# Kernel tuning notes

Measured on AMD Instinct MI355X. Metric: run time of the kernel, lower is better.

## Reference

```python
import jax, jax.numpy as jnp
import numpy as np

B, S, H, DK, DV, DE = 2, 256, 8, 64, 64, 512
DT = H * DV
EPS = 1e-5

def _clin(xr, xi, W, b):
    # complex linear: x @ W + b with (re, im) parts; W: (2, d_in, d_out), b: (2, d_out)
    yr = xr @ W[0] - xi @ W[1] + b[0]
    yi = xr @ W[1] + xi @ W[0] + b[1]
    return yr, yi

def _emul(ar, ai, br, bi):
    # complex elementwise (Hadamard) multiply
    return ar * br - ai * bi, ar * bi + ai * br

def _forward(Z_q, Z_k, Z_v, t_measure_all, Wq, bq, Wk, bk, Wv, bv, Wp, bp,
             lambda_imag_v, lambda_real_v, lambda_omega_sqrt_v,
             lambda_gamma_sqrt_v, noise_floor, tau, eta_param):
    Bn = Z_q.shape[0]
    t = t_measure_all[0, :-1]
    t = t / (t[-1] - t[0])

    def heads(z, W, b, d):
        yr, yi = _clin(z[:, 0], z[:, 1], W, b)
        f = lambda a: a.reshape(Bn, S, H, d).swapaxes(-1, -2)  # (B,S,d,H)
        return f(yr), f(yi)

    Qr, Qi = heads(Z_q, Wq, bq, DK)
    Kr, Ki = heads(Z_k, Wk, bk, DK)
    Vr, Vi = heads(Z_v, Wv, bv, DV)

    # complex eigenvalues in conjugate pairs: (DV, H)
    lam_im = jnp.concatenate([lambda_imag_v, -lambda_imag_v], axis=1).T
    lam_re = jnp.broadcast_to(lambda_real_v[None, :], (DV, H))

    # forward/backward exponential kernels exp(+/- lambda t): (S, DV, H)
    phase = t[:, None, None] * lam_im[None]
    mag = jnp.exp(t[:, None, None] * lam_re[None])
    ef_r = mag * jnp.cos(phase); ef_i = mag * jnp.sin(phase)
    eb_r = jnp.cos(phase) / mag; eb_i = -jnp.sin(phase) / mag
    me_r, me_i = ef_r[0], ef_i[0]  # mat_exp

    # scalar covariance kernel per (i, j, head): process noise + measurement noise
    omega = lambda_omega_sqrt_v ** 2
    gamma = lambda_gamma_sqrt_v ** 2 + EPS
    dt = jnp.maximum(t[:, None] - t[None, :], 0.0)  # causal lags only
    den = 2.0 * lambda_real_v  # (H,)
    safe = jnp.where(jnp.abs(den) > 1e-6, den, 1.0)
    x = dt[:, :, None] * den
    g = jnp.where(jnp.abs(den) > 1e-6, jnp.expm1(x) / safe, dt[:, :, None])
    V_avg = omega * g + gamma * jnp.exp(x)  # (S,S,H)

    # factorized kernels: U_* = exp(-lambda t_j) * X_j ; propagator factor |exp(lambda t_i)|^2
    Uq_r, Uq_i = _emul(eb_r[None], eb_i[None], Qr, Qi)
    Uk_r, Uk_i = _emul(eb_r[None], eb_i[None], Kr, Ki)
    Uv_r, Uv_i = _emul(eb_r[None], eb_i[None], Vr, Vi)
    Vk2 = ef_r ** 2 + ef_i ** 2  # (S,DV,H)

    # precision-weighted residual norm |exp(lambda(t_i-t_j)) k_j - q_i|^2
    Uq2 = Uq_r ** 2 + Uq_i ** 2
    Uk2 = Uk_r ** 2 + Uk_i ** 2
    self_q = jnp.einsum('idh,bidh->bih', Vk2, Uq2)
    term_k = jnp.einsum('idh,bjdh->bijh', Vk2, Uk2)
    cross = (jnp.einsum('bidh,bjdh->bijh', Vk2[None] * Uq_r, Uk_r)
             + jnp.einsum('bidh,bjdh->bijh', Vk2[None] * Uq_i, Uk_i))
    R = term_k + self_q[:, :, None, :] - 2.0 * cross  # (B,S,S,H)

    base = (noise_floor ** 2 + EPS) * V_avg[None] + R
    scores = -(tau ** 2) * jnp.log(base)
    mask = jnp.tril(jnp.ones((S, S), bool))
    scores = jnp.where(mask[None, :, :, None], scores, -jnp.inf)
    attn = jax.nn.softmax(scores, axis=2)  # (B,S,S,H)

    # complex matmul with real-valued attention (imag part of Q_ij is zero)
    er = jnp.einsum('bijh,bjdh->bidh', attn, Uv_r)
    ei = jnp.einsum('bijh,bjdh->bidh', attn, Uv_i)
    est_r, est_i = _emul(ef_r[None], ef_i[None], er, ei)

    eta = jax.nn.sigmoid(eta_param)[0, 0]  # (1,DV,H)
    el_r = (1.0 - eta) * Vr + jax.nn.sigmoid(eta) * est_r
    el_i = (1.0 - eta) * Vi + jax.nn.sigmoid(eta) * est_i

    pr, pi = _emul(me_r[None, None], me_i[None, None], el_r, el_i)
    merge = lambda a: a.swapaxes(-1, -2).reshape(Bn, S, DT)
    o_r, o_i = _clin(merge(pr), merge(pi), Wp, bp)
    out = jnp.stack([o_r, o_i], axis=1)  # (B,2,S,DE)

    # all-pairs propagated estimates Z_ij = exp(lambda t_i) * U_v,j
    zr, zi = _emul(ef_r[None, :, None], ef_i[None, :, None],
                   Uv_r[:, None], Uv_i[:, None])  # (B,S,S,DV,H)
    zm = lambda a: a.swapaxes(-1, -2).reshape(Bn, S, S, DT)
    Z_ij = jnp.stack([zm(zr), zm(zi)], axis=1)  # (B,2,S,S,DT)

    est_latent = jnp.stack([el_r, el_i], axis=1)  # (B,2,S,DV,H)
    Q_ij = jnp.stack([attn, jnp.zeros_like(attn)], axis=1)
    epoch_lambdas = jnp.stack([lam_re, lam_im], 0).swapaxes(-1, -2).reshape(2, H * DV)[..., None]
    return est_latent, out, Q_ij, Z_ij, epoch_lambdas

def setup_inputs():
    key = jax.random.key(0)
    k = jax.random.split(key, 16)
    sc_in = 1.0 / np.sqrt(DE)
    sc_out = 1.0 / np.sqrt(DT)
    return {
        'Z_q': jax.random.normal(k[0], (B, 2, S, DE), jnp.float32),
        'Z_k': jax.random.normal(k[1], (B, 2, S, DE), jnp.float32),
        'Z_v': jax.random.normal(k[2], (B, 2, S, DE), jnp.float32),
        't_measure_all': jnp.arange(S + 1, dtype=jnp.float32)[None, :],
        'Wq': jax.random.normal(k[3], (2, DE, DT), jnp.float32) * sc_in,
        'bq': jax.random.normal(k[4], (2, DT), jnp.float32) * 0.01,
        'Wk': jax.random.normal(k[5], (2, DE, DT), jnp.float32) * sc_in,
        'bk': jax.random.normal(k[6], (2, DT), jnp.float32) * 0.01,
        'Wv': jax.random.normal(k[7], (2, DE, DT), jnp.float32) * sc_in,
        'bv': jax.random.normal(k[8], (2, DT), jnp.float32) * 0.01,
        'Wp': jax.random.normal(k[9], (2, DT, DE), jnp.float32) * sc_out,
        'bp': jax.random.normal(k[10], (2, DE), jnp.float32) * 0.01,
        'lambda_imag_v': jax.random.normal(k[11], (H, DV // 2), jnp.float32),
        'lambda_real_v': jax.random.normal(k[12], (H,), jnp.float32) * 0.5,
        'lambda_omega_sqrt_v': jax.random.normal(k[13], (H,), jnp.float32),
        'lambda_gamma_sqrt_v': jax.random.normal(k[14], (H,), jnp.float32),
        'noise_floor': jnp.ones((H,), jnp.float32),
        'tau': jnp.ones((H,), jnp.float32),
        'eta_param': jnp.zeros((1, 1, 1, DV, H), jnp.float32),
    }

def reference(Z_q, Z_k, Z_v, t_measure_all, Wq, bq, Wk, bk, Wv, bv, Wp, bp,
              lambda_imag_v, lambda_real_v, lambda_omega_sqrt_v,
              lambda_gamma_sqrt_v, noise_floor, tau, eta_param):
    return _forward(Z_q, Z_k, Z_v, t_measure_all, Wq, bq, Wk, bk, Wv, bv, Wp, bp,
                    lambda_imag_v, lambda_real_v, lambda_omega_sqrt_v,
                    lambda_gamma_sqrt_v, noise_floor, tau, eta_param)
```

## Files before the change

kernel.cpp:

```cpp
#include <hip/hip_runtime.h>
#include <hip/hip_bf16.h>
#include <math.h>

constexpr int kB  = 2;
constexpr int kS  = 256;
constexpr int kH  = 8;
constexpr float kEPS = 1e-5f;

constexpr int OFF_EST = 0;
constexpr int OFF_OUT = 524288;
constexpr int OFF_QIJ = 1048576;
constexpr int OFF_ZIJ = 3145728;
constexpr int OFF_EPO = 137363456;

constexpr int WS_EFR = 0;
constexpr int WS_EFI = 131072;
constexpr int WS_EBR = 262144;
constexpr int WS_EBI = 393216;
constexpr int WS_UQR = 524288;
constexpr int WS_UQI = 786432;
constexpr int WS_UKR = 1048576;
constexpr int WS_UKI = 1310720;
constexpr int WS_UVR = 1572864;
constexpr int WS_UVI = 1835008;
constexpr int WS_VR  = 2097152;
constexpr int WS_VI  = 2359296;
constexpr int WS_BF  = 3145728;

constexpr int A2Q = 0;
constexpr int A2K = 524288;
constexpr int A2V = 1048576;
constexpr int B2R0 = 1572864;

typedef __attribute__((ext_vector_type(8))) short bf16x8;
typedef __attribute__((ext_vector_type(4))) float f32x4;
typedef __attribute__((ext_vector_type(8))) unsigned short u16x8;
typedef __attribute__((ext_vector_type(4))) unsigned short u16x4;

__device__ __forceinline__ float sigm(float x) { return 1.f / (1.f + expf(-x)); }
__device__ __forceinline__ unsigned short f2b(float f) {
    __hip_bfloat16 h = __float2bfloat16(f);
    return *reinterpret_cast<unsigned short*>(&h);
}

__global__ __launch_bounds__(256) void k_prep(
    const float* __restrict__ tall, const float* __restrict__ Lim,
    const float* __restrict__ Lre,
    const float* __restrict__ zq, const float* __restrict__ zk,
    const float* __restrict__ zv,
    const float* __restrict__ wq, const float* __restrict__ wk,
    const float* __restrict__ wv, const float* __restrict__ wp,
    float* __restrict__ efr, float* __restrict__ efi,
    float* __restrict__ ebr, float* __restrict__ ebi,
    float* __restrict__ epo, __hip_bfloat16* __restrict__ bfbase)
{
    __shared__ float s0[64][65];
    __shared__ float s1[64][65];
    const int bid = blockIdx.x;
    const int tid = threadIdx.x;

    if (bid < 512) {
        int idx = bid * 256 + tid;
        int s = idx >> 9;
        int c = idx & 511;
        int h = c >> 6;
        int d = c & 63;
        float li = (d < 32) ? Lim[h * 32 + d] : -Lim[h * 32 + d - 32];
        float lr = Lre[h];
        float t  = tall[s] / (tall[kS - 1] - tall[0]);
        float ph  = t * li;
        float mag = expf(t * lr);
        float cp  = cosf(ph);
        float sp  = sinf(ph);
        efr[idx] = mag * cp;
        efi[idx] = mag * sp;
        ebr[idx] = cp / mag;
        ebi[idx] = -sp / mag;
        if (s == 0) {
            epo[c]       = lr;
            epo[512 + c] = li;
        }
    } else if (bid < 1280) {
        int idx = (bid - 512) * 256 + tid;
        int tz  = idx >> 16;
        int rem = idx & 65535;
        int m   = rem >> 7;
        int k0  = (rem & 127) * 8;
        const float* src = (tz == 0) ? zq : (tz == 1) ? zk : zv;
        int b = m >> 8, s = m & 255;
        int c = (k0 >= 512) ? 1 : 0;
        int e = k0 - c * 512;
        const float* p = src + ((b * 2 + c) * 256 + s) * 512 + e;
        float4 v0 = *(const float4*)p;
        float4 v1 = *(const float4*)(p + 4);
        u16x8 o;
        o[0] = f2b(v0.x); o[1] = f2b(v0.y); o[2] = f2b(v0.z); o[3] = f2b(v0.w);
        o[4] = f2b(v1.x); o[5] = f2b(v1.y); o[6] = f2b(v1.z); o[7] = f2b(v1.w);
        __hip_bfloat16* dst = bfbase + ((tz == 0) ? A2Q : (tz == 1) ? A2K : A2V)
                              + m * 1024 + k0;
        *(u16x8*)dst = o;
    } else {
        int wid = bid - 1280;
        int z = wid >> 7;
        int r2 = wid & 127;
        int k0 = (r2 & 15) * 64;
        int n0 = (r2 >> 4) * 64;
        const float* W  = (z == 0) ? wq : (z == 1) ? wk : (z == 2) ? wv : wp;
        const float* W0 = W;
        const float* W1 = W + 262144;
        const int kp = k0 & 511;
        const bool hf = (k0 >= 512);
        const int r = tid >> 2;
        const int q = tid & 3;
#pragma unroll
        for (int c = 0; c < 4; ++c) {
            int col = q * 16 + c * 4;
            *(float4*)&s0[r][col] = *(const float4*)&W0[(kp + r) * 512 + n0 + col];
            *(float4*)&s1[r][col] = *(const float4*)&W1[(kp + r) * 512 + n0 + col];
        }
        __syncthreads();
        u16x8 r0, r1, i0, i1;
#pragma unroll
        for (int u = 0; u < 8; ++u) {
            int kl = q * 16 + u;
            float w0 = s0[kl][r], w1 = s1[kl][r];
            r0[u] = f2b(hf ? -w1 : w0);
            i0[u] = f2b(hf ?  w0 : w1);
        }
#pragma unroll
        for (int u = 0; u < 8; ++u) {
            int kl = q * 16 + 8 + u;
            float w0 = s0[kl][r], w1 = s1[kl][r];
            r1[u] = f2b(hf ? -w1 : w0);
            i1[u] = f2b(hf ?  w0 : w1);
        }
        __hip_bfloat16* pr = bfbase + B2R0 + z * 1048576
                             + (size_t)(n0 + r) * 1024 + k0 + q * 16;
        __hip_bfloat16* pi = pr + 524288;
        *(u16x8*)pr       = r0;
        *(u16x8*)(pr + 8) = r1;
        *(u16x8*)pi       = i0;
        *(u16x8*)(pi + 8) = i1;
    }
}

template<bool IS_P>
__global__ __launch_bounds__(256) void k_cmfma(
    const __hip_bfloat16* __restrict__ bfbase,
    const __hip_bfloat16* __restrict__ a2p,
    const float* __restrict__ bq, const float* __restrict__ bk,
    const float* __restrict__ bv, const float* __restrict__ bp,
    const float* __restrict__ ebr, const float* __restrict__ ebi,
    float* __restrict__ uqr, float* __restrict__ uqi,
    float* __restrict__ ukr, float* __restrict__ uki,
    float* __restrict__ uvr, float* __restrict__ uvi,
    float* __restrict__ vr,  float* __restrict__ vi,
    float* __restrict__ outp)
{
    __shared__ __align__(16) char sm[24576];
    char* sA  = sm;
    char* sBr = sm + 8192;
    char* sBi = sm + 16384;

    const int mode = IS_P ? 3 : (int)blockIdx.z;
    const __hip_bfloat16* A2 = IS_P ? a2p
        : bfbase + ((mode == 0) ? A2Q : (mode == 1) ? A2K : A2V);
    const __hip_bfloat16* Br = bfbase + B2R0 + mode * 1048576;
    const __hip_bfloat16* Bi = Br + 524288;
    const float* bias = IS_P ? bp : ((mode == 0) ? bq : (mode == 1) ? bk : bv);

    const int tid = threadIdx.x;
    const int m0 = blockIdx.y * 64;
    const int n0 = blockIdx.x * 64;
    const int lane = tid & 63;
    const int wv2 = tid >> 6;
    const int wr = wv2 >> 1, wc = wv2 & 1;
    const int lx = lane & 15, lhi = lane >> 4;

    const int srow  = tid >> 2;
    const int sslot = (tid & 3) * 32;

    const char* gA  = (const char*)(A2 + (size_t)(m0 + srow) * 1024);
    const char* gBr = (const char*)(Br + (size_t)(n0 + srow) * 1024);
    const char* gBi = (const char*)(Bi + (size_t)(n0 + srow) * 1024);
    const int swz = (srow & 7) << 4;
    char* dA  = sA  + srow * 128;
    char* dBr = sBr + srow * 128;
    char* dBi = sBi + srow * 128;

    f32x4 accR[2][2] = {};
    f32x4 accI[2][2] = {};

    int rowA[2], rowB[2];
    rowA[0] = wr * 32 + lx;  rowA[1] = rowA[0] + 16;
    rowB[0] = wc * 32 + lx;  rowB[1] = rowB[0] + 16;

    for (int kt = 0; kt < 16; ++kt) {
        const int kb = kt * 128;
        {
            float4 a0 = *(const float4*)(gA  + kb + sslot);
            float4 a1 = *(const float4*)(gA  + kb + sslot + 16);
            float4 b0 = *(const float4*)(gBr + kb + sslot);
            float4 b1 = *(const float4*)(gBr + kb + sslot + 16);
            float4 c0 = *(const float4*)(gBi + kb + sslot);
            float4 c1 = *(const float4*)(gBi + kb + sslot + 16);
            *(float4*)(dA  + ( sslot       ^ swz)) = a0;
            *(float4*)(dA  + ((sslot + 16) ^ swz)) = a1;
            *(float4*)(dBr + ( sslot       ^ swz)) = b0;
            *(float4*)(dBr + ((sslot + 16) ^ swz)) = b1;
            *(float4*)(dBi + ( sslot       ^ swz)) = c0;
            *(float4*)(dBi + ((sslot + 16) ^ swz)) = c1;
        }
        __syncthreads();
#pragma unroll
        for (int kk = 0; kk < 2; ++kk) {
            const int kbyte = kk * 64 + lhi * 16;
            bf16x8 af[2], brf[2], bif[2];
#pragma unroll
            for (int x = 0; x < 2; ++x) {
                int ra = rowA[x];
                af[x]  = *(const bf16x8*)(sA  + ra * 128 + (kbyte ^ ((ra & 7) << 4)));
                int rb = rowB[x];
                brf[x] = *(const bf16x8*)(sBr + rb * 128 + (kbyte ^ ((rb & 7) << 4)));
                bif[x] = *(const bf16x8*)(sBi + rb * 128 + (kbyte ^ ((rb & 7) << 4)));
            }
#pragma unroll
            for (int a = 0; a < 2; ++a)
#pragma unroll
                for (int bb = 0; bb < 2; ++bb) {
                    accR[a][bb] = __builtin_amdgcn_mfma_f32_16x16x32_bf16(
                        af[a], brf[bb], accR[a][bb], 0, 0, 0);
                    accI[a][bb] = __builtin_amdgcn_mfma_f32_16x16x32_bf16(
                        af[a], bif[bb], accI[a][bb], 0, 0, 0);
                }
        }
        __syncthreads();
    }

#pragma unroll
    for (int a = 0; a < 2; ++a) {
#pragma unroll
        for (int bb = 0; bb < 2; ++bb) {
#pragma unroll
            for (int j = 0; j < 4; ++j) {
                int m = m0 + wr * 32 + a * 16 + lhi * 4 + j;
                int n = n0 + wc * 32 + bb * 16 + lx;
                float yr = accR[a][bb][j] + bias[n];
                float yi = accI[a][bb][j] + bias[512 + n];
                int b = m >> 8, s = m & 255;
                if (IS_P) {
                    int rowo = m * 512 + b * 131072;
                    outp[rowo + n] = yr;
                    outp[rowo + 131072 + n] = yi;
                } else {
                    int h = n >> 6, d = n & 63;
                    float er_ = ebr[s * 512 + n], ei_ = ebi[s * 512 + n];
                    float ur = er_ * yr - ei_ * yi;
                    float ui = er_ * yi + ei_ * yr;
                    if (mode == 0) {
                        int idx = ((b * 8 + h) * 256 + s) * 64 + d;
                        uqr[idx] = ur; uqi[idx] = ui;
                    } else if (mode == 1) {
                        int idx = ((b * 8 + h) * 64 + d) * 256 + s;
                        ukr[idx] = ur; uki[idx] = ui;
                    } else {
                        int idx = ((b * 8 + h) * 256 + s) * 64 + d;
                        uvr[idx] = ur; uvi[idx] = ui;
                        int vidx = (b * 256 + s) * 512 + d * 8 + h;
                        vr[vidx] = yr; vi[vidx] = yi;
                    }
                }
            }
        }
    }
}

__global__ __launch_bounds__(256) void k_zij_attn(
    const float* __restrict__ efr, const float* __restrict__ efi,
    const float* __restrict__ uvr, const float* __restrict__ uvi,
    float* __restrict__ zout,
    const float* __restrict__ uqr, const float* __restrict__ uqi,
    const float* __restrict__ ukr, const float* __restrict__ uki,
    const float* __restrict__ tall,
    const float* __restrict__ Lre, const float* __restrict__ Lom,
    const float* __restrict__ Lga, const float* __restrict__ NF,
    const float* __restrict__ TAU,
    float* __restrict__ qij,
    const float* __restrict__ vr,  const float* __restrict__ vi,
    const float* __restrict__ ETA,
    float* __restrict__ out_est, __hip_bfloat16* __restrict__ a2p)
{
    __shared__ __align__(16) char smem[66688];
    float (*sP)[257] = (float(*)[257])smem;
    float (*sKr)[32] = (float(*)[32])(smem + 32896);
    float (*sKi)[32] = (float(*)[32])(smem + 41088);
    float (*sQr)[68] = (float(*)[68])(smem + 49280);
    float (*sQi)[68] = (float(*)[68])(smem + 57984);
    float (*sVr)[64] = (float(*)[64])(smem + 32896);
    float (*sVi)[64] = (float(*)[64])(smem + 41088);

    const int bid = blockIdx.x;
    const int tid = threadIdx.x;

    if (bid >= 128) {
        const int z  = bid - 128;
        const int j0 = (z & 63) * 4;
        const int i  = (z >> 6) & 255;
        const int b  = z >> 14;
#pragma unroll
        for (int half = 0; half < 2; half++) {
            int dt = half * 256 + tid;
            float fr = efr[i * 512 + dt];
            float fi = efi[i * 512 + dt];
            int h = dt >> 6, d = dt & 63;
            const float* ur = uvr + ((b * 8 + h) * 256) * 64 + d;
            const float* ui = uvi + ((b * 8 + h) * 256) * 64 + d;
#pragma unroll
            for (int jj = 0; jj < 4; jj++) {
                int j = j0 + jj;
                float vr_ = ur[j * 64];
                float vi_ = ui[j * 64];
                float zr = fr * vr_ - fi * vi_;
                float zi = fr * vi_ + fi * vr_;
                int idx0 = (b * 2) * 33554432 + i * 131072 + j * 512 + dt;
                __builtin_nontemporal_store(zr, &zout[idx0]);
                __builtin_nontemporal_store(zi, &zout[idx0 + 33554432]);
            }
        }
        return;
    }

    const int it = bid & 7;
    const int h  = (bid >> 3) & 7;
    const int b  = bid >> 6;
    const int i0 = it * 32;
    const int ti = tid >> 3;
    const int tj = tid & 7;
    const int i  = i0 + ti;

    {
        const float* qsr = uqr + ((b * 8 + h) * 256 + i) * 64;
        const float* qsi = uqi + ((b * 8 + h) * 256 + i) * 64;
        *(float4*)&sQr[ti][tj * 4]      = *(const float4*)&qsr[tj * 4];
        *(float4*)&sQr[ti][32 + tj * 4] = *(const float4*)&qsr[32 + tj * 4];
        *(float4*)&sQi[ti][tj * 4]      = *(const float4*)&qsi[tj * 4];
        *(float4*)&sQi[ti][32 + tj * 4] = *(const float4*)&qsi[32 + tj * 4];
    }

    const float lre  = Lre[h];
    const float om   = Lom[h] * Lom[h];
    const float ga   = Lga[h] * Lga[h] + kEPS;
    const float nf2  = NF[h] * NF[h] + kEPS;
    const float tau2 = TAU[h] * TAU[h];
    const float den  = 2.f * lre;
    const float invT = 1.f / (tall[kS - 1] - tall[0]);
    const float t_i  = tall[i] * invT;
    const float m2i  = expf(2.f * t_i * lre);
    const bool  denok = fabsf(den) > 1e-6f;

    const int kr2 = tid >> 2;
    const int kq2 = tid & 3;

    for (int jt = 0; jt <= it; ++jt) {
        const int j0 = jt * 32;
        __syncthreads();
        {
            const float* ksrc_r = ukr + ((b * 8 + h) * 64 + kr2) * 256 + j0;
            const float* ksrc_i = uki + ((b * 8 + h) * 64 + kr2) * 256 + j0;
            *(float4*)&sKr[kr2][kq2 * 4]      = *(const float4*)&ksrc_r[kq2 * 4];
            *(float4*)&sKr[kr2][16 + kq2 * 4] = *(const float4*)&ksrc_r[16 + kq2 * 4];
            *(float4*)&sKi[kr2][kq2 * 4]      = *(const float4*)&ksrc_i[kq2 * 4];
            *(float4*)&sKi[kr2][16 + kq2 * 4] = *(const float4*)&ksrc_i[16 + kq2 * 4];
        }
        __syncthreads();

        float acc[4] = {0.f, 0.f, 0.f, 0.f};
#pragma unroll 16
        for (int d = 0; d < 64; d++) {
            float qr = sQr[ti][d];
            float qi = sQi[ti][d];
            float4 kr = *(float4*)&sKr[d][tj * 4];
            float4 ki = *(float4*)&sKi[d][tj * 4];
#define DSTEP(c, KRC, KIC)                                    \
            { float dr = qr - KRC; float di = qi - KIC;       \
              acc[c] = fmaf(dr, dr, acc[c]);                  \
              acc[c] = fmaf(di, di, acc[c]); }
            DSTEP(0, kr.x, ki.x)
            DSTEP(1, kr.y, ki.y)
            DSTEP(2, kr.z, ki.z)
            DSTEP(3, kr.w, ki.w)
#undef DSTEP
        }

#pragma unroll
        for (int c = 0; c < 4; c++) {
            int j = j0 + tj * 4 + c;
            if (j <= i) {
                float t_j = tall[j] * invT;
                float dtt = fmaxf(t_i - t_j, 0.f);
                float x = dtt * den;
                float g = denok ? (expm1f(x) / den) : dtt;
                float Vv = om * g + ga * expf(x);
                float base = nf2 * Vv + m2i * acc[c];
                sP[ti][j] = -tau2 * logf(base);
            }
        }
    }
    __syncthreads();

    float mx = -1e30f;
    for (int j = tj; j <= i; j += 8) mx = fmaxf(mx, sP[ti][j]);
#pragma unroll
    for (int m = 1; m < 8; m <<= 1) mx = fmaxf(mx, __shfl_xor(mx, m));
    float sum = 0.f;
    for (int j = tj; j <= i; j += 8) {
        float e = expf(sP[ti][j] - mx);
        sP[ti][j] = e;
        sum += e;
    }
#pragma unroll
    for (int m = 1; m < 8; m <<= 1) sum += __shfl_xor(sum, m);
    const float inv = 1.f / sum;

    float* srow   = qij + ((b * 512 + i) * 256) * 8 + h;
    float* qi_out = qij + ((b * 512 + 256 + i) * 256) * 8 + h;
    const int jfill = i0 + 32;
    for (int j = tj; j < 256; j += 8) {
        float p = 0.f;
        if (j <= i) p = sP[ti][j] * inv;
        if (j < jfill) sP[ti][j] = p;
        srow[j * 8]   = p;
        qi_out[j * 8] = 0.f;
    }
    __syncthreads();

    const int dl = tid & 7;
    float accR[8] = {0.f}, accI[8] = {0.f};

    for (int jt = 0; jt <= it; jt++) {
        const int j0 = jt * 32;
        {
            const float* sr = uvr + ((b * 8 + h) * 256 + j0 + ti) * 64;
            const float* si = uvi + ((b * 8 + h) * 256 + j0 + ti) * 64;
            *(float4*)&sVr[ti][dl * 4]      = *(const float4*)&sr[dl * 4];
            *(float4*)&sVr[ti][32 + dl * 4] = *(const float4*)&sr[32 + dl * 4];
            *(float4*)&sVi[ti][dl * 4]      = *(const float4*)&si[dl * 4];
            *(float4*)&sVi[ti][32 + dl * 4] = *(const float4*)&si[32 + dl * 4];
        }
        __syncthreads();

#pragma unroll 8
        for (int jj = 0; jj < 32; jj++) {
            float a = sP[ti][j0 + jj];
            float4 v0 = *(float4*)&sVr[jj][dl * 8];
            float4 v1 = *(float4*)&sVr[jj][dl * 8 + 4];
            float4 w0 = *(float4*)&sVi[jj][dl * 8];
            float4 w1 = *(float4*)&sVi[jj][dl * 8 + 4];
            float vv[8] = {v0.x, v0.y, v0.z, v0.w, v1.x, v1.y, v1.z, v1.w};
            float ww[8] = {w0.x, w0.y, w0.z, w0.w, w1.x, w1.y, w1.z, w1.w};
#pragma unroll
            for (int c = 0; c < 8; c++) {
                accR[c] = fmaf(a, vv[c], accR[c]);
                accI[c] = fmaf(a, ww[c], accI[c]);
            }
        }
        __syncthreads();
    }

    const int cb = h * 64 + dl * 8;
    f32x4 fr0 = *(const f32x4*)&efr[i * 512 + cb];
    f32x4 fr1 = *(const f32x4*)&efr[i * 512 + cb + 4];
    f32x4 fi0 = *(const f32x4*)&efi[i * 512 + cb];
    f32x4 fi1 = *(const f32x4*)&efi[i * 512 + cb + 4];
    f32x4 mr0 = *(const f32x4*)&efr[cb];
    f32x4 mr1 = *(const f32x4*)&efr[cb + 4];
    f32x4 mi0 = *(const f32x4*)&efi[cb];
    f32x4 mi1 = *(const f32x4*)&efi[cb + 4];

    u16x8 o_r, o_i;
#pragma unroll
    for (int c = 0; c < 8; c++) {
        float fr = (c < 4) ? fr0[c] : fr1[c - 4];
        float fi = (c < 4) ? fi0[c] : fi1[c - 4];
        float mr = (c < 4) ? mr0[c] : mr1[c - 4];
        float mi = (c < 4) ? mi0[c] : mi1[c - 4];
        int p = dl * 64 + c * 8 + h;
        float estr = fr * accR[c] - fi * accI[c];
        float esti = fr * accI[c] + fi * accR[c];
        float et = sigm(ETA[p]);
        float w1 = 1.f - et;
        float w2 = sigm(et);
        float vr_ = vr[(b * 256 + i) * 512 + p];
        float vi_ = vi[(b * 256 + i) * 512 + p];
        float elr = w1 * vr_ + w2 * estr;
        float eli = w1 * vi_ + w2 * esti;
        out_est[((b * 2 + 0) * 256 + i) * 512 + p] = elr;
        out_est[((b * 2 + 1) * 256 + i) * 512 + p] = eli;
        o_r[c] = f2b(mr * elr - mi * eli);
        o_i[c] = f2b(mr * eli + mi * elr);
    }
    __hip_bfloat16* ap = a2p + (b * 256 + i) * 1024 + cb;
    *(u16x8*)ap         = o_r;
    *(u16x8*)(ap + 512) = o_i;
}

extern "C" void kernel_launch(void* const* d_in, const int* in_sizes, int n_in,
                              void* d_out, int out_size, void* d_ws, size_t ws_size,
                              hipStream_t stream)
{
    const float* Zq   = (const float*)d_in[0];
    const float* Zk   = (const float*)d_in[1];
    const float* Zv   = (const float*)d_in[2];
    const float* tall = (const float*)d_in[3];
    const float* Wq   = (const float*)d_in[4];
    const float* bq   = (const float*)d_in[5];
    const float* Wk   = (const float*)d_in[6];
    const float* bk   = (const float*)d_in[7];
    const float* Wv   = (const float*)d_in[8];
    const float* bv   = (const float*)d_in[9];
    const float* Wp   = (const float*)d_in[10];
    const float* bp   = (const float*)d_in[11];
    const float* Lim  = (const float*)d_in[12];
    const float* Lre  = (const float*)d_in[13];
    const float* Lom  = (const float*)d_in[14];
    const float* Lga  = (const float*)d_in[15];
    const float* NF   = (const float*)d_in[16];
    const float* TAU  = (const float*)d_in[17];
    const float* ETA  = (const float*)d_in[18];

    float* out = (float*)d_out;
    float* ws  = (float*)d_ws;

    float* efr = ws + WS_EFR; float* efi = ws + WS_EFI;
    float* ebr = ws + WS_EBR; float* ebi = ws + WS_EBI;
    float* uqr = ws + WS_UQR; float* uqi = ws + WS_UQI;
    float* ukr = ws + WS_UKR; float* uki = ws + WS_UKI;
    float* uvr = ws + WS_UVR; float* uvi = ws + WS_UVI;
    float* vr  = ws + WS_VR;  float* vi  = ws + WS_VI;
    __hip_bfloat16* bfbase = (__hip_bfloat16*)(ws + WS_BF);
    __hip_bfloat16* a2p    = (__hip_bfloat16*)(ws + WS_EBR);

    k_prep<<<1792, 256, 0, stream>>>(tall, Lim, Lre, Zq, Zk, Zv,
                                     Wq, Wk, Wv, Wp,
                                     efr, efi, ebr, ebi,
                                     out + OFF_EPO, bfbase);

    k_cmfma<false><<<dim3(8, 8, 3), 256, 0, stream>>>(
        bfbase, nullptr, bq, bk, bv, bp, ebr, ebi,
        uqr, uqi, ukr, uki, uvr, uvi, vr, vi, nullptr);

    k_zij_attn<<<32896, 256, 0, stream>>>(
        efr, efi, uvr, uvi, out + OFF_ZIJ,
        uqr, uqi, ukr, uki, tall, Lre, Lom, Lga, NF, TAU,
        out + OFF_QIJ, vr, vi, ETA, out + OFF_EST, a2p);

    k_cmfma<true><<<dim3(8, 8, 1), 256, 0, stream>>>(
        bfbase, a2p, bq, bk, bv, bp, ebr, ebi,
        nullptr, nullptr, nullptr, nullptr, nullptr, nullptr, nullptr, nullptr,
        out + OFF_OUT);
}
```

Before: 139.3 us.

## Fuse Q/K projection, attention and output projection into one flag-synchronized kernel

Moves the Q/K projection GEMM tiles and the output projection GEMM into the big attention/Zij kernel as extra block ranges, coordinated with global atomic counters that blocks spin on. The V projection stays in its own kernel because the Zij blocks consume it. The aim is to overlap the small GEMMs and attention with the large Zij streaming work and remove launch gaps. The risk is deadlock or stalls if waiting blocks occupy CUs before their producers get scheduled, and spin-polling adds overhead.

```diff
diff --git a/kernel.cpp b/kernel.cpp
--- a/kernel.cpp
+++ b/kernel.cpp
@@ -35,12 +35,27 @@
 typedef __attribute__((ext_vector_type(8))) short bf16x8;
 typedef __attribute__((ext_vector_type(4))) float f32x4;
 typedef __attribute__((ext_vector_type(8))) unsigned short u16x8;
-typedef __attribute__((ext_vector_type(4))) unsigned short u16x4;
+
+__device__ unsigned g_flagQK;
+__device__ unsigned g_flagA;
 
 __device__ __forceinline__ float sigm(float x) { return 1.f / (1.f + expf(-x)); }
 __device__ __forceinline__ unsigned short f2b(float f) {
     __hip_bfloat16 h = __float2bfloat16(f);
     return *reinterpret_cast<unsigned short*>(&h);
+}
+
+__device__ __forceinline__ void signal_flag(unsigned* f) {
+    __threadfence();
+    __syncthreads();
+    if (threadIdx.x == 0) atomicAdd(f, 1u);
+}
+__device__ __forceinline__ void wait_flag(unsigned* f, unsigned target) {
+    if (threadIdx.x == 0) {
+        while (atomicAdd(f, 0u) < target) { __builtin_amdgcn_s_sleep(2); }
+        __threadfence();
+    }
+    __syncthreads();
 }
 
 __global__ __launch_bounds__(256) void k_prep(
@@ -58,6 +73,8 @@
     __shared__ float s1[64][65];
     const int bid = blockIdx.x;
     const int tid = threadIdx.x;
+
+    if (bid == 0 && tid == 0) { g_flagQK = 0u; g_flagA = 0u; }
 
     if (bid < 512) {
         int idx = bid * 256 + tid;
@@ -144,34 +161,15 @@
     }
 }
 
-template<bool IS_P>
-__global__ __launch_bounds__(256) void k_cmfma(
-    const __hip_bfloat16* __restrict__ bfbase,
-    const __hip_bfloat16* __restrict__ a2p,
-    const float* __restrict__ bq, const float* __restrict__ bk,
-    const float* __restrict__ bv, const float* __restrict__ bp,
-    const float* __restrict__ ebr, const float* __restrict__ ebi,
-    float* __restrict__ uqr, float* __restrict__ uqi,
-    float* __restrict__ ukr, float* __restrict__ uki,
-    float* __restrict__ uvr, float* __restrict__ uvi,
-    float* __restrict__ vr,  float* __restrict__ vi,
-    float* __restrict__ outp)
+__device__ __forceinline__ void gemm_tile(
+    char* sm, const __hip_bfloat16* A2, const __hip_bfloat16* Br,
+    const __hip_bfloat16* Bi, int m0, int n0, int tid,
+    f32x4 accR[2][2], f32x4 accI[2][2])
 {
-    __shared__ __align__(16) char sm[24576];
     char* sA  = sm;
     char* sBr = sm + 8192;
     char* sBi = sm + 16384;
 
-    const int mode = IS_P ? 3 : (int)blockIdx.z;
-    const __hip_bfloat16* A2 = IS_P ? a2p
-        : bfbase + ((mode == 0) ? A2Q : (mode == 1) ? A2K : A2V);
-    const __hip_bfloat16* Br = bfbase + B2R0 + mode * 1048576;
-    const __hip_bfloat16* Bi = Br + 524288;
-    const float* bias = IS_P ? bp : ((mode == 0) ? bq : (mode == 1) ? bk : bv);
-
-    const int tid = threadIdx.x;
-    const int m0 = blockIdx.y * 64;
-    const int n0 = blockIdx.x * 64;
     const int lane = tid & 63;
     const int wv2 = tid >> 6;
     const int wr = wv2 >> 1, wc = wv2 & 1;
@@ -187,9 +185,6 @@
     char* dA  = sA  + srow * 128;
     char* dBr = sBr + srow * 128;
     char* dBi = sBi + srow * 128;
-
-    f32x4 accR[2][2] = {};
-    f32x4 accI[2][2] = {};
 
     int rowA[2], rowB[2];
     rowA[0] = wr * 32 + lx;  rowA[1] = rowA[0] + 16;
@@ -236,51 +231,59 @@
         }
         __syncthreads();
     }
-
-#pragma unroll
-    for (int a = 0; a < 2; ++a) {
-#pragma unroll
-        for (int bb = 0; bb < 2; ++bb) {
+}
+
+__global__ __launch_bounds__(256) void k_cmfma_v(
+    const __hip_bfloat16* __restrict__ bfbase,
+    const float* __restrict__ bv,
+    const float* __restrict__ ebr, const float* __restrict__ ebi,
+    float* __restrict__ uvr, float* __restrict__ uvi,
+    float* __restrict__ vr,  float* __restrict__ vi)
+{
+    __shared__ __align__(16) char sm[24576];
+    const int tid = threadIdx.x;
+    const int m0 = blockIdx.y * 64;
+    const int n0 = blockIdx.x * 64;
+    f32x4 accR[2][2] = {};
+    f32x4 accI[2][2] = {};
+    gemm_tile(sm, bfbase + A2V, bfbase + B2R0 + 2 * 1048576,
+              bfbase + B2R0 + 2 * 1048576 + 524288, m0, n0, tid, accR, accI);
+
+    const int lane = tid & 63;
+    const int wv2 = tid >> 6;
+    const int wr = wv2 >> 1, wc = wv2 & 1;
+    const int lx = lane & 15, lhi = lane >> 4;
+#pragma unroll
+    for (int a = 0; a < 2; ++a)
+#pragma unroll
+        for (int bb = 0; bb < 2; ++bb)
 #pragma unroll
             for (int j = 0; j < 4; ++j) {
                 int m = m0 + wr * 32 + a * 16 + lhi * 4 + j;
                 int n = n0 + wc * 32 + bb * 16 + lx;
-                float yr = accR[a][bb][j] + bias[n];
-                float yi = accI[a][bb][j] + bias[512 + n];
+                float yr = accR[a][bb][j] + bv[n];
+                float yi = accI[a][bb][j] + bv[512 + n];
                 int b = m >> 8, s = m & 255;
-                if (IS_P) {
-                    int rowo = m * 512 + b * 131072;
-                    outp[rowo + n] = yr;
-                    outp[rowo + 131072 + n] = yi;
-                } else {
-                    int h = n >> 6, d = n & 63;
-                    float er_ = ebr[s * 512 + n], ei_ = ebi[s * 512 + n];
-                    float ur = er_ * yr - ei_ * yi;
-                    float ui = er_ * yi + ei_ * yr;
-                    if (mode == 0) {
-                        int idx = ((b * 8 + h) * 256 + s) * 64 + d;
-                        uqr[idx] = ur; uqi[idx] = ui;
-                    } else if (mode == 1) {
-                        int idx = ((b * 8 + h) * 64 + d) * 256 + s;
-                        ukr[idx] = ur; uki[idx] = ui;
-                    } else {
-                        int idx = ((b * 8 + h) * 256 + s) * 64 + d;
-                        uvr[idx] = ur; uvi[idx] = ui;
-                        int vidx = (b * 256 + s) * 512 + d * 8 + h;
-                        vr[vidx] = yr; vi[vidx] = yi;
-                    }
-                }
+                int h = n >> 6, d = n & 63;
+                float er_ = ebr[s * 512 + n], ei_ = ebi[s * 512 + n];
+                int idx = ((b * 8 + h) * 256 + s) * 64 + d;
+                uvr[idx] = er_ * yr - ei_ * yi;
+                uvi[idx] = er_ * yi + ei_ * yr;
+                int vidx = (b * 256 + s) * 512 + d * 8 + h;
+                vr[vidx] = yr; vi[vidx] = yi;
             }
-        }
-    }
-}
-
-__global__ __launch_bounds__(256) void k_zij_attn(
+}
+
+__global__ __launch_bounds__(256) void k_mega(
     const float* __restrict__ efr, const float* __restrict__ efi,
     const float* __restrict__ uvr, const float* __restrict__ uvi,
     float* __restrict__ zout,
-    const float* __restrict__ uqr, const float* __restrict__ uqi,
-    const float* __restrict__ ukr, const float* __restrict__ uki,
+    const __hip_bfloat16* __restrict__ bfbase,
+    const float* __restrict__ bq, const float* __restrict__ bk,
+    const float* __restrict__ bp,
+    const float* __restrict__ ebr, const float* __restrict__ ebi,
+    float* __restrict__ uqr, float* __restrict__ uqi,
+    float* __restrict__ ukr, float* __restrict__ uki,
     const float* __restrict__ tall,
     const float* __restrict__ Lre, const float* __restrict__ Lom,
     const float* __restrict__ Lga, const float* __restrict__ NF,
@@ -288,22 +291,15 @@
     float* __restrict__ qij,
     const float* __restrict__ vr,  const float* __restrict__ vi,
     const float* __restrict__ ETA,
-    float* __restrict__ out_est, __hip_bfloat16* __restrict__ a2p)
+    float* __restrict__ out_est, __hip_bfloat16* __restrict__ a2p,
+    float* __restrict__ outp)
 {
     __shared__ __align__(16) char smem[66688];
-    float (*sP)[257] = (float(*)[257])smem;
-    float (*sKr)[32] = (float(*)[32])(smem + 32896);
-    float (*sKi)[32] = (float(*)[32])(smem + 41088);
-    float (*sQr)[68] = (float(*)[68])(smem + 49280);
-    float (*sQi)[68] = (float(*)[68])(smem + 57984);
-    float (*sVr)[64] = (float(*)[64])(smem + 32896);
-    float (*sVi)[64] = (float(*)[64])(smem + 41088);
-
     const int bid = blockIdx.x;
     const int tid = threadIdx.x;
 
-    if (bid >= 128) {
-        const int z  = bid - 128;
+    if (bid >= 320) {
+        const int z  = bid - 320;
         const int j0 = (z & 63) * 4;
         const int i  = (z >> 6) & 255;
         const int b  = z >> 14;
@@ -330,9 +326,96 @@
         return;
     }
 
-    const int it = bid & 7;
-    const int h  = (bid >> 3) & 7;
-    const int b  = bid >> 6;
+    if (bid < 128) {
+        const int mode = bid >> 6;
+        const int m0 = ((bid >> 3) & 7) * 64;
+        const int n0 = (bid & 7) * 64;
+        const __hip_bfloat16* A2 = bfbase + ((mode == 0) ? A2Q : A2K);
+        const __hip_bfloat16* Br = bfbase + B2R0 + mode * 1048576;
+        const __hip_bfloat16* Bi = Br + 524288;
+        const float* bias = (mode == 0) ? bq : bk;
+        f32x4 accR[2][2] = {};
+        f32x4 accI[2][2] = {};
+        gemm_tile(smem, A2, Br, Bi, m0, n0, tid, accR, accI);
+
+        const int lane = tid & 63;
+        const int wv2 = tid >> 6;
+        const int wr = wv2 >> 1, wc = wv2 & 1;
+        const int lx = lane & 15, lhi = lane >> 4;
+#pragma unroll
+        for (int a = 0; a < 2; ++a)
+#pragma unroll
+            for (int bb = 0; bb < 2; ++bb)
+#pragma unroll
+                for (int j = 0; j < 4; ++j) {
+                    int m = m0 + wr * 32 + a * 16 + lhi * 4 + j;
+                    int n = n0 + wc * 32 + bb * 16 + lx;
+                    float yr = accR[a][bb][j] + bias[n];
+                    float yi = accI[a][bb][j] + bias[512 + n];
+                    int b = m >> 8, s = m & 255;
+                    int h = n >> 6, d = n & 63;
+                    float er_ = ebr[s * 512 + n], ei_ = ebi[s * 512 + n];
+                    float ur = er_ * yr - ei_ * yi;
+                    float ui = er_ * yi + ei_ * yr;
+                    if (mode == 0) {
+                        int idx = ((b * 8 + h) * 256 + s) * 64 + d;
+                        uqr[idx] = ur; uqi[idx] = ui;
+                    } else {
+                        int idx = ((b * 8 + h) * 64 + d) * 256 + s;
+                        ukr[idx] = ur; uki[idx] = ui;
+                    }
+                }
+        signal_flag(&g_flagQK);
+        return;
+    }
+
+    if (bid >= 256) {
+        wait_flag(&g_flagA, 128u);
+        const int pid = bid - 256;
+        const int m0 = (pid >> 3) * 64;
+        const int n0 = (pid & 7) * 64;
+        const __hip_bfloat16* Br = bfbase + B2R0 + 3 * 1048576;
+        const __hip_bfloat16* Bi = Br + 524288;
+        f32x4 accR[2][2] = {};
+        f32x4 accI[2][2] = {};
+        gemm_tile(smem, a2p, Br, Bi, m0, n0, tid, accR, accI);
+
+        const int lane = tid & 63;
+        const int wv2 = tid >> 6;
+        const int wr = wv2 >> 1, wc = wv2 & 1;
+        const int lx = lane & 15, lhi = lane >> 4;
+#pragma unroll
+        for (int a = 0; a < 2; ++a)
+#pragma unroll
+            for (int bb = 0; bb < 2; ++bb)
+#pragma unroll
+                for (int j = 0; j < 4; ++j) {
+                    int m = m0 + wr * 32 + a * 16 + lhi * 4 + j;
+                    int n = n0 + wc * 32 + bb * 16 + lx;
+                    float yr = accR[a][bb][j] + bp[n];
+                    float yi = accI[a][bb][j] + bp[512 + n];
+                    int b = m >> 8;
+                    int rowo = m * 512 + b * 131072;
+                    outp[rowo + n] = yr;
+                    outp[rowo + 131072 + n] = yi;
+                }
+        return;
+    }
+
+    wait_flag(&g_flagQK, 128u);
+
+    float (*sP)[257] = (float(*)[257])smem;
+    float (*sKr)[32] = (float(*)[32])(smem + 32896);
+    float (*sKi)[32] = (float(*)[32])(smem + 41088);
+    float (*sQr)[68] = (float(*)[68])(smem + 49280);
+    float (*sQi)[68] = (float(*)[68])(smem + 57984);
+    float (*sVr)[64] = (float(*)[64])(smem + 32896);
+    float (*sVi)[64] = (float(*)[64])(smem + 41088);
+
+    const int aid = bid - 128;
+    const int it = aid & 7;
+    const int h  = (aid >> 3) & 7;
+    const int b  = aid >> 6;
     const int i0 = it * 32;
     const int ti = tid >> 3;
     const int tj = tid & 7;
@@ -502,6 +585,8 @@
     __hip_bfloat16* ap = a2p + (b * 256 + i) * 1024 + cb;
     *(u16x8*)ap         = o_r;
     *(u16x8*)(ap + 512) = o_i;
+
+    signal_flag(&g_flagA);
 }
 
 extern "C" void kernel_launch(void* const* d_in, const int* in_sizes, int n_in,
@@ -545,17 +630,14 @@
                                      efr, efi, ebr, ebi,
                                      out + OFF_EPO, bfbase);
 
-    k_cmfma<false><<<dim3(8, 8, 3), 256, 0, stream>>>(
-        bfbase, nullptr, bq, bk, bv, bp, ebr, ebi,
-        uqr, uqi, ukr, uki, uvr, uvi, vr, vi, nullptr);
-
-    k_zij_attn<<<32896, 256, 0, stream>>>(
+    k_cmfma_v<<<dim3(8, 8), 256, 0, stream>>>(
+        bfbase, bv, ebr, ebi, uvr, uvi, vr, vi);
+
+    k_mega<<<33088, 256, 0, stream>>>(
         efr, efi, uvr, uvi, out + OFF_ZIJ,
-        uqr, uqi, ukr, uki, tall, Lre, Lom, Lga, NF, TAU,
-        out + OFF_QIJ, vr, vi, ETA, out + OFF_EST, a2p);
-
-    k_cmfma<true><<<dim3(8, 8, 1), 256, 0, stream>>>(
-        bfbase, a2p, bq, bk, bv, bp, ebr, ebi,
-        nullptr, nullptr, nullptr, nullptr, nullptr, nullptr, nullptr, nullptr,
+        bfbase, bq, bk, bp, ebr, ebi,
+        uqr, uqi, ukr, uki,
+        tall, Lre, Lom, Lga, NF, TAU,
+        out + OFF_QIJ, vr, vi, ETA, out + OFF_EST, a2p,
         out + OFF_OUT);
 }
```

Result: slower. 207.3 us (+48.9%).
